# Performance work log

Hardware: AMD Instinct MI355X
Metric: run time of the kernel (lower is better)

The kernel has to match this reference:

```python
import jax, jax.numpy as jnp
import numpy as np
import math

N, E, C, A, M, B, H = 50000, 600000, 32, 32, 32, 10, 64


def setup_inputs() -> dict:
    key = jax.random.key(0)
    ks = jax.random.split(key, 14)
    f = jnp.float32
    node_input = jax.random.normal(ks[0], (N, C), f)
    node_attr = jax.random.normal(ks[1], (N, A), f)
    node_deg = 1.0 + 31.0 * jax.random.uniform(ks[2], (N, 1), dtype=f)  # degrees >= 1
    edge_src = jax.random.randint(ks[3], (E,), 0, N, jnp.int32)
    edge_dst = jax.random.randint(ks[4], (E,), 0, N, jnp.int32)
    edge_attr = jax.random.normal(ks[5], (E, 9), f)  # SH up to lmax=2: 1+3+5
    edge_length_embedded = jax.random.uniform(ks[6], (E, B), dtype=f)
    w_lin_in = jax.random.normal(ks[7], (C, A, C), f)    # FCTP(Cx0e, Ax0e -> Cx0e)
    w_lin_mask = jax.random.normal(ks[8], (C, A, M), f)  # FCTP scalar block of linear_mask
    w_out0 = jax.random.normal(ks[9], (C, A, M), f)      # linear_output, l=0 block
    w_out1 = jax.random.normal(ks[10], (C, A, M), f)     # l=1 block
    w_out2 = jax.random.normal(ks[11], (C, A, M), f)     # l=2 block
    W0 = jax.random.normal(ks[12], (B, H), f)            # radial net (edge2weight)
    W1 = jax.random.normal(ks[13], (H, 3 * C), f)        # -> tensor_edge.weight_numel = 3C ('uvu', v=1)
    return dict(node_input=node_input, node_attr=node_attr, node_deg=node_deg,
                edge_src=edge_src, edge_dst=edge_dst, edge_attr=edge_attr,
                edge_length_embedded=edge_length_embedded,
                w_lin_in=w_lin_in, w_lin_mask=w_lin_mask,
                w_out0=w_out0, w_out1=w_out1, w_out2=w_out2, W0=W0, W1=W1,
                numb=100, n=8)


def reference(node_input, node_attr, node_deg, edge_src, edge_dst, edge_attr,
              edge_length_embedded, w_lin_in, w_lin_mask, w_out0, w_out1, w_out2,
              W0, W1, numb, n):
    # GraphConvolution.forward with irreps_in=Cx0e, irreps_node_attr=Ax0e,
    # irreps_edge_attr=1x0e+1x1o+1x2e (lmax=2), irreps_out=Mx0e+Mx1o+Mx2e.
    nN = node_input.shape[0]
    inv_ca = 1.0 / math.sqrt(C * A)

    def fctp_scalar(x, z, w):  # FullyConnectedTensorProduct with all-scalar in1/in2
        return jnp.einsum('nu,nv,uvk->nk', x, z, w) * inv_ca

    # linear_input, then node_deg normalization
    h0 = fctp_scalar(node_input, node_attr, w_lin_in)            # [N, C]
    deg_isqrt = 1.0 / jnp.sqrt(node_deg)                          # [N, 1]
    nf = h0 * deg_isqrt
    # linear_mask: only 0e outputs have tp paths (scalars x scalars); 1o/2e are zero
    mask_scalar = fctp_scalar(node_input, node_attr, w_lin_mask)  # [N, M]

    # edge2weight radial MLP (e3nn FullyConnectedNet style: /sqrt(fan_in), silu hidden)
    h = jax.nn.silu(edge_length_embedded @ W0 * (1.0 / math.sqrt(B)))
    ew = h @ W1 * (1.0 / math.sqrt(H))                            # [E, 3C]
    w0e, w1o, w2e = ew[:, :C], ew[:, C:2 * C], ew[:, 2 * C:]

    # tensor_edge: 'uvu' 0e(x)l->l paths: out[u,m] = w[u]*x_src[u]*Y_l[m]
    xs = nf[edge_src]                                             # gather [E, C]
    m0 = (w0e * xs) * edge_attr[:, :1]                            # [E, C]
    m1 = (w1o * xs)[:, :, None] * edge_attr[:, None, 1:4]         # [E, C, 3]
    m2 = (w2e * xs)[:, :, None] * edge_attr[:, None, 4:9]         # [E, C, 5]

    # scatter-reduce to destination nodes, then deg normalization
    a0 = jax.ops.segment_sum(m0, edge_dst, num_segments=nN) * deg_isqrt
    a1 = jax.ops.segment_sum(m1, edge_dst, num_segments=nN) * deg_isqrt[:, :, None]
    a2 = jax.ops.segment_sum(m2, edge_dst, num_segments=nN) * deg_isqrt[:, :, None]

    # linear_output: FCTP(mid, Ax0e -> out); scalar attr mixes multiplicities per l
    out0 = jnp.einsum('nu,nv,uvk->nk', a0, node_attr, w_out0) * inv_ca        # [N, M]
    out1 = jnp.einsum('num,nv,uvk->nkm', a1, node_attr, w_out1) * inv_ca      # [N, M, 3]
    out2 = jnp.einsum('num,nv,uvk->nkm', a2, node_attr, w_out2) * inv_ca      # [N, M, 5]

    # c_s * node_mask + c_x * node_output; output_mask is 1 on 0e, 0 on 1o/2e
    c_s, c_x = math.sin(math.pi / 8), math.cos(math.pi / 8)
    scal = c_s * mask_scalar + c_x * out0
    return jnp.concatenate([scal, out1.reshape(nN, 3 * M), out2.reshape(nN, 5 * M)], axis=1)
```

## Files before the change

### kernel.cpp

```cpp
#include <hip/hip_runtime.h>

#define NC 32
#define NA 32
#define NB 10
#define NH 64

typedef __attribute__((ext_vector_type(8))) short bf16x8;
typedef __attribute__((ext_vector_type(4))) float f32x4;

static __device__ __forceinline__ unsigned short f2bf(float f) {
  union { float f; unsigned u; } v; v.f = f;
  unsigned r = v.u + 0x7fffu + ((v.u >> 16) & 1u);
  return (unsigned short)(r >> 16);
}
static __device__ __forceinline__ float bf2f(unsigned short b) {
  union { unsigned u; float f; } v; v.u = ((unsigned)b) << 16;
  return v.f;
}

__global__ void k_prep(const float* __restrict__ nattr, const float* __restrict__ ndeg,
                       const float* __restrict__ w0, const float* __restrict__ w1,
                       const float* __restrict__ w2, const float* __restrict__ w3,
                       const float* __restrict__ w4, const float* __restrict__ W1g,
                       unsigned short* __restrict__ zb, float* __restrict__ dis,
                       unsigned short* __restrict__ wrp, unsigned short* __restrict__ w1p,
                       int N) {
  int i = blockIdx.x * 256 + threadIdx.x;
  int nz = N * NC;
  if (i < nz) { zb[i] = f2bf(nattr[i]); return; }
  i -= nz;
  if (i < N) { dis[i] = rsqrtf(ndeg[i]); return; }
  i -= N;
  if (i < 5 * 32768) {
    int T = i >> 15, r = i & 32767;
    int t = r >> 9, l = (r >> 3) & 63, b = r & 7;
    int j = t * 16 + (l & 15);
    int u = j >> 5, k = j & 31, v = 8 * (l >> 4) + b;
    const float* w = (T == 0) ? w0 : (T == 1) ? w1 : (T == 2) ? w2 : (T == 3) ? w3 : w4;
    wrp[T * 32768 + (t * 64 + l) * 8 + b] = f2bf(w[u * 1024 + v * 32 + k] * (1.0f / 32.0f));
    return;
  }
  i -= 5 * 32768;
  if (i < 6144) {
    int c = i / 3072, r2 = i % 3072;
    int t = r2 >> 9, l = (r2 >> 3) & 63, b = r2 & 7;
    int k = 32 * c + 8 * (l >> 4) + b, col = 16 * t + (l & 15);
    w1p[i] = f2bf(W1g[k * 96 + col] * 0.125f);
  }
}

__global__ __launch_bounds__(512) void k_fctp(
    const unsigned short* __restrict__ wrp, const unsigned short* __restrict__ zb,
    const float* __restrict__ xp, int nm, int xnstr, int xoff,
    float* __restrict__ outp, int onstr,
    const float* __restrict__ scalep,
    const float* __restrict__ addp, float selfc, float addc) {
  __shared__ float zw[16 * 1025];
  __shared__ float xl[16][5][32];
  int tid = threadIdx.x;
  int lane = tid & 63, wv = tid >> 6;
  int nbase = blockIdx.x << 4;

  for (int i = tid; i < 16 * nm * 32; i += 512) {
    int n = i / (nm * 32); int rem = i - n * (nm * 32); int m = rem >> 5, u = rem & 31;
    xl[n][m][u] = xp[(nbase + n) * xnstr + xoff + m * 32 + u];
  }

  bf16x8 af = *(const bf16x8*)(zb + (nbase + (lane & 15)) * 32 + 8 * (lane >> 4));
  f32x4 acc[8];
#pragma unroll
  for (int i2 = 0; i2 < 8; ++i2) {
    int t = wv * 8 + i2;
    bf16x8 bfr = *(const bf16x8*)(wrp + (t * 64 + lane) * 8);
    f32x4 z4 = {0.f, 0.f, 0.f, 0.f};
    acc[i2] = __builtin_amdgcn_mfma_f32_16x16x32_bf16(af, bfr, z4, 0, 0, 0);
  }
  int rb = 4 * (lane >> 4);
#pragma unroll
  for (int i2 = 0; i2 < 8; ++i2) {
    int col = (wv * 8 + i2) * 16 + (lane & 15);
#pragma unroll
    for (int r = 0; r < 4; ++r) zw[(rb + r) * 1025 + col] = acc[i2][r];
  }
  __syncthreads();

  int n = tid >> 5, k = tid & 31;
  float sc = scalep ? scalep[nbase + n] : 1.0f;
  const float* zr = &zw[n * 1025];
  for (int m = 0; m < nm; ++m) {
    float s = 0.f;
#pragma unroll
    for (int u = 0; u < 32; ++u) s = fmaf(xl[n][m][u], zr[u * 32 + k], s);
    s *= sc;
    if (addp) s = selfc * s + addc * addp[(nbase + n) * 32 + k];
    outp[(nbase + n) * onstr + k * nm + m] = s;
  }
}

__global__ void k_count(const int* __restrict__ dst, int* __restrict__ cnt, int E) {
  int i = blockIdx.x * 256 + threadIdx.x;
  if (i < E) atomicAdd(&cnt[dst[i]], 1);
}
__global__ __launch_bounds__(512) void k_scan1(const int* __restrict__ cnt, int* __restrict__ exl,
                                               int* __restrict__ bsum, int n) {
  __shared__ int s[512];
  int t = threadIdx.x;
  int i = blockIdx.x * 512 + t;
  int v = (i < n) ? cnt[i] : 0;
  s[t] = v;
  __syncthreads();
  for (int off = 1; off < 512; off <<= 1) {
    int add = (t >= off) ? s[t - off] : 0;
    __syncthreads();
    s[t] += add;
    __syncthreads();
  }
  if (i < n) exl[i] = s[t] - v;
  if (t == 511) bsum[blockIdx.x] = s[511];
}
__global__ void k_scan2(int* __restrict__ bsum, int nb) {
  __shared__ int s[128];
  int t = threadIdx.x;
  int v = (t < nb) ? bsum[t] : 0;
  s[t] = v;
  __syncthreads();
  for (int off = 1; off < 128; off <<= 1) {
    int add = (t >= off) ? s[t - off] : 0;
    __syncthreads();
    s[t] += add;
    __syncthreads();
  }
  if (t < nb) bsum[t] = s[t] - v;
}
__global__ void k_scan3(int* __restrict__ off, const int* __restrict__ bbase,
                        int* __restrict__ cur, int N, int E) {
  int i = blockIdx.x * 256 + threadIdx.x;
  if (i < N) {
    int o = off[i] + bbase[i >> 9];
    off[i] = o;
    cur[i] = o;
  } else if (i == N) {
    off[N] = E;
  }
}
__global__ void k_fill(const int* __restrict__ dst, int* __restrict__ cur,
                       int* __restrict__ eid, int E) {
  int i = blockIdx.x * 256 + threadIdx.x;
  if (i < E) {
    int pos = atomicAdd(&cur[dst[i]], 1);
    eid[pos] = i;
  }
}

__global__ __launch_bounds__(256) void k_mlp(const float* __restrict__ el,
                                             const float* __restrict__ W0g,
                                             const unsigned short* __restrict__ w1p,
                                             unsigned short* __restrict__ ew, int E) {
  __shared__ float w0s[NB * NH];
  int tid = threadIdx.x;
  for (int i = tid; i < NB * NH; i += 256) w0s[i] = W0g[i] * 0.31622776601683794f;
  __syncthreads();
  int lane = tid & 63, wv = tid >> 6;
  int ebase = blockIdx.x * 64 + wv * 16;
  int erow = ebase + (lane & 15);
  float elr[NB];
#pragma unroll
  for (int b = 0; b < NB; ++b) elr[b] = el[erow * NB + b];
  int g8 = 8 * (lane >> 4);
  bf16x8 afr[2];
#pragma unroll
  for (int c = 0; c < 2; ++c) {
#pragma unroll
    for (int b = 0; b < 8; ++b) {
      int j = 32 * c + g8 + b;
      float p = 0.f;
#pragma unroll
      for (int q = 0; q < NB; ++q) p = fmaf(elr[q], w0s[q * NH + j], p);
      float h = p / (1.f + __expf(-p));
      afr[c][b] = (short)f2bf(h);
    }
  }
  f32x4 acc[6];
#pragma unroll
  for (int t = 0; t < 6; ++t) { f32x4 z4 = {0.f, 0.f, 0.f, 0.f}; acc[t] = z4; }
#pragma unroll
  for (int c = 0; c < 2; ++c) {
#pragma unroll
    for (int t = 0; t < 6; ++t) {
      bf16x8 bfr = *(const bf16x8*)(w1p + ((c * 6 + t) * 64 + lane) * 8);
      acc[t] = __builtin_amdgcn_mfma_f32_16x16x32_bf16(afr[c], bfr, acc[t], 0, 0, 0);
    }
  }
  int rb = 4 * (lane >> 4);
#pragma unroll
  for (int t = 0; t < 6; ++t) {
    int col = 16 * t + (lane & 15);
#pragma unroll
    for (int r = 0; r < 4; ++r) {
      int e = ebase + rb + r;
      ew[e * 96 + col] = f2bf(acc[t][r]);
    }
  }
}

__global__ __launch_bounds__(256) void k_gather(
    const int* __restrict__ off, const int* __restrict__ eid, const int* __restrict__ esrc,
    const float* __restrict__ eattr, const unsigned short* __restrict__ ew,
    const float* __restrict__ nf, const float* __restrict__ dis,
    float* __restrict__ a_all, int N) {
  int hw = (blockIdx.x * 256 + threadIdx.x) >> 5;
  int u = threadIdx.x & 31;
  if (hw >= N) return;
  int beg = off[hw], end = off[hw + 1];
  float a0 = 0, a1x = 0, a1y = 0, a1z = 0, b0 = 0, b1 = 0, b2 = 0, b3 = 0, b4 = 0;
  for (int p = beg; p < end; ++p) {
    int e = eid[p];
    int s = esrc[e];
    float xs = nf[s * 32 + u];
    const unsigned short* ewr = ew + e * 96;
    float w0 = bf2f(ewr[u]), w1 = bf2f(ewr[32 + u]), w2 = bf2f(ewr[64 + u]);
    const float* ea = eattr + e * 9;
    float t0 = w0 * xs, t1 = w1 * xs, t2 = w2 * xs;
    a0  = fmaf(t0, ea[0], a0);
    a1x = fmaf(t1, ea[1], a1x);
    a1y = fmaf(t1, ea[2], a1y);
    a1z = fmaf(t1, ea[3], a1z);
    b0  = fmaf(t2, ea[4], b0);
    b1  = fmaf(t2, ea[5], b1);
    b2  = fmaf(t2, ea[6], b2);
    b3  = fmaf(t2, ea[7], b3);
    b4  = fmaf(t2, ea[8], b4);
  }
  float d = dis[hw];
  float* ar = a_all + hw * 288;
  ar[0 * 32 + u] = a0 * d;
  ar[1 * 32 + u] = a1x * d;
  ar[2 * 32 + u] = a1y * d;
  ar[3 * 32 + u] = a1z * d;
  ar[4 * 32 + u] = b0 * d;
  ar[5 * 32 + u] = b1 * d;
  ar[6 * 32 + u] = b2 * d;
  ar[7 * 32 + u] = b3 * d;
  ar[8 * 32 + u] = b4 * d;
}

extern "C" void kernel_launch(void* const* d_in, const int* in_sizes, int n_in,
                              void* d_out, int out_size, void* d_ws, size_t ws_size,
                              hipStream_t stream) {
  const float* node_input = (const float*)d_in[0];
  const float* node_attr  = (const float*)d_in[1];
  const float* node_deg   = (const float*)d_in[2];
  const int*   edge_src   = (const int*)d_in[3];
  const int*   edge_dst   = (const int*)d_in[4];
  const float* edge_attr  = (const float*)d_in[5];
  const float* el_emb     = (const float*)d_in[6];
  const float* w_lin_in   = (const float*)d_in[7];
  const float* w_lin_mask = (const float*)d_in[8];
  const float* w_out0     = (const float*)d_in[9];
  const float* w_out1     = (const float*)d_in[10];
  const float* w_out2     = (const float*)d_in[11];
  const float* W0         = (const float*)d_in[12];
  const float* W1         = (const float*)d_in[13];
  int N = in_sizes[0] / 32;
  int E = in_sizes[3];
  float* out = (float*)d_out;

  char* p = (char*)d_ws;
  auto carve = [&](size_t bytes) { char* r = p; p += (bytes + 255) & ~(size_t)255; return r; };
  unsigned short* ew  = (unsigned short*)carve((size_t)E * 96 * 2);
  float* a_all        = (float*)carve((size_t)N * 288 * 4);
  float* nf           = (float*)carve((size_t)N * 32 * 4);
  float* maskb        = (float*)carve((size_t)N * 32 * 4);
  unsigned short* zb  = (unsigned short*)carve((size_t)N * 32 * 2);
  float* dis          = (float*)carve((size_t)N * 4);
  unsigned short* wrp = (unsigned short*)carve(5 * 32768 * 2);
  unsigned short* w1p = (unsigned short*)carve(6144 * 2);
  int* cnt            = (int*)carve((size_t)N * 4);
  int* off            = (int*)carve((size_t)(N + 1) * 4);
  int* cur            = (int*)carve((size_t)N * 4);
  int* eid            = (int*)carve((size_t)E * 4);
  int* bsum           = (int*)carve(1024);

  hipMemsetAsync(cnt, 0, (size_t)N * 4, stream);

  int tot = N * 32 + N + 5 * 32768 + 6144;
  k_prep<<<(tot + 255) / 256, 256, 0, stream>>>(node_attr, node_deg, w_lin_in, w_lin_mask,
                                                w_out0, w_out1, w_out2, W1, zb, dis, wrp, w1p, N);

  const float c_s = 0.3826834323650898f;
  const float c_x = 0.9238795325112867f;
  int nblk = N / 16;

  k_fctp<<<nblk, 512, 0, stream>>>(wrp + 0 * 32768, zb, node_input, 1, 32, 0, nf, 32,
                                   dis, nullptr, 0.f, 0.f);
  k_fctp<<<nblk, 512, 0, stream>>>(wrp + 1 * 32768, zb, node_input, 1, 32, 0, maskb, 32,
                                   nullptr, nullptr, 0.f, 0.f);

  k_count<<<(E + 255) / 256, 256, 0, stream>>>(edge_dst, cnt, E);
  int nb1 = (N + 511) / 512;
  k_scan1<<<nb1, 512, 0, stream>>>(cnt, off, bsum, N);
  k_scan2<<<1, 128, 0, stream>>>(bsum, nb1);
  k_scan3<<<(N + 1 + 255) / 256, 256, 0, stream>>>(off, bsum, cur, N, E);
  k_fill<<<(E + 255) / 256, 256, 0, stream>>>(edge_dst, cur, eid, E);

  k_mlp<<<E / 64, 256, 0, stream>>>(el_emb, W0, w1p, ew, E);
  k_gather<<<(N * 32 + 255) / 256, 256, 0, stream>>>(off, eid, edge_src, edge_attr, ew, nf,
                                                     dis, a_all, N);

  k_fctp<<<nblk, 512, 0, stream>>>(wrp + 2 * 32768, zb, a_all, 1, 288, 0, out + 0, 288,
                                   nullptr, maskb, c_x, c_s);
  k_fctp<<<nblk, 512, 0, stream>>>(wrp + 3 * 32768, zb, a_all, 3, 288, 32, out + 32, 288,
                                   nullptr, nullptr, 0.f, 0.f);
  k_fctp<<<nblk, 512, 0, stream>>>(wrp + 4 * 32768, zb, a_all, 5, 288, 128, out + 128, 288,
                                   nullptr, nullptr, 0.f, 0.f);
}
```

Before: 456.4 us.

## Scatter edge weights and attributes into CSR order in MLP kernel

The fill kernel now records each edge's CSR position, and the edge MLP kernel stages its bf16 output in shared memory before writing it, together with edge_src and edge_attr, into dst-sorted order. The gather kernel then reads edge data contiguously by CSR position instead of through an indirection, and it also prefetches the next source node feature. This removes the random eid-indexed loads from the gather at the cost of scattered writes in the MLP kernel and extra workspace for the permuted edge_src and edge_attr arrays.

After: 488.6 us. 1.07x slower.

```diff
diff --git a/kernel.cpp b/kernel.cpp
--- a/kernel.cpp
+++ b/kernel.cpp
@@ -144,25 +144,42 @@
   }
 }
 __global__ void k_fill(const int* __restrict__ dst, int* __restrict__ cur,
-                       int* __restrict__ eid, int E) {
+                       int* __restrict__ pos, int E) {
   int i = blockIdx.x * 256 + threadIdx.x;
   if (i < E) {
-    int pos = atomicAdd(&cur[dst[i]], 1);
-    eid[pos] = i;
+    pos[i] = atomicAdd(&cur[dst[i]], 1);
   }
 }
 
 __global__ __launch_bounds__(256) void k_mlp(const float* __restrict__ el,
                                              const float* __restrict__ W0g,
                                              const unsigned short* __restrict__ w1p,
-                                             unsigned short* __restrict__ ew, int E) {
+                                             const int* __restrict__ pos,
+                                             const int* __restrict__ esrc,
+                                             const float* __restrict__ eattr,
+                                             unsigned short* __restrict__ ewP,
+                                             int* __restrict__ esrcP,
+                                             float* __restrict__ eattrP, int E) {
   __shared__ float w0s[NB * NH];
+  __shared__ __align__(16) unsigned short tile[64 * 104];
+  __shared__ int posl[64];
   int tid = threadIdx.x;
+  int ebase = blockIdx.x * 64;
   for (int i = tid; i < NB * NH; i += 256) w0s[i] = W0g[i] * 0.31622776601683794f;
-  __syncthreads();
+  if (tid < 64) posl[tid] = pos[ebase + tid];
+  __syncthreads();
+
+  for (int i = tid; i < 64 * 10; i += 256) {
+    int le = i / 10, c = i - le * 10;
+    int p = posl[le];
+    int e = ebase + le;
+    if (c == 0) esrcP[p] = esrc[e];
+    else eattrP[(size_t)p * 9 + (c - 1)] = eattr[(size_t)e * 9 + (c - 1)];
+  }
+
   int lane = tid & 63, wv = tid >> 6;
-  int ebase = blockIdx.x * 64 + wv * 16;
-  int erow = ebase + (lane & 15);
+  int eloc0 = wv * 16;
+  int erow = ebase + eloc0 + (lane & 15);
   float elr[NB];
 #pragma unroll
   for (int b = 0; b < NB; ++b) elr[b] = el[erow * NB + b];
@@ -197,15 +214,21 @@
     int col = 16 * t + (lane & 15);
 #pragma unroll
     for (int r = 0; r < 4; ++r) {
-      int e = ebase + rb + r;
-      ew[e * 96 + col] = f2bf(acc[t][r]);
+      tile[(eloc0 + rb + r) * 104 + col] = f2bf(acc[t][r]);
     }
   }
+  __syncthreads();
+  for (int ch = tid; ch < 64 * 12; ch += 256) {
+    int le = ch / 12, seg = ch - le * 12;
+    int p = posl[le];
+    *(uint4*)(ewP + (size_t)p * 96 + seg * 8) =
+        *(const uint4*)(&tile[le * 104 + seg * 8]);
+  }
 }
 
 __global__ __launch_bounds__(256) void k_gather(
-    const int* __restrict__ off, const int* __restrict__ eid, const int* __restrict__ esrc,
-    const float* __restrict__ eattr, const unsigned short* __restrict__ ew,
+    const int* __restrict__ off, const int* __restrict__ esrcP,
+    const float* __restrict__ eattrP, const unsigned short* __restrict__ ewP,
     const float* __restrict__ nf, const float* __restrict__ dis,
     float* __restrict__ a_all, int N) {
   int hw = (blockIdx.x * 256 + threadIdx.x) >> 5;
@@ -213,13 +236,20 @@
   if (hw >= N) return;
   int beg = off[hw], end = off[hw + 1];
   float a0 = 0, a1x = 0, a1y = 0, a1z = 0, b0 = 0, b1 = 0, b2 = 0, b3 = 0, b4 = 0;
+  float xs_next = 0.f;
+  if (beg < end) {
+    int s0 = esrcP[beg];
+    xs_next = nf[(size_t)s0 * 32 + u];
+  }
   for (int p = beg; p < end; ++p) {
-    int e = eid[p];
-    int s = esrc[e];
-    float xs = nf[s * 32 + u];
-    const unsigned short* ewr = ew + e * 96;
+    float xs = xs_next;
+    if (p + 1 < end) {
+      int s2 = esrcP[p + 1];
+      xs_next = nf[(size_t)s2 * 32 + u];
+    }
+    const unsigned short* ewr = ewP + (size_t)p * 96;
     float w0 = bf2f(ewr[u]), w1 = bf2f(ewr[32 + u]), w2 = bf2f(ewr[64 + u]);
-    const float* ea = eattr + e * 9;
+    const float* ea = eattrP + (size_t)p * 9;
     float t0 = w0 * xs, t1 = w1 * xs, t2 = w2 * xs;
     a0  = fmaf(t0, ea[0], a0);
     a1x = fmaf(t1, ea[1], a1x);
@@ -232,7 +262,7 @@
     b4  = fmaf(t2, ea[8], b4);
   }
   float d = dis[hw];
-  float* ar = a_all + hw * 288;
+  float* ar = a_all + (size_t)hw * 288;
   ar[0 * 32 + u] = a0 * d;
   ar[1 * 32 + u] = a1x * d;
   ar[2 * 32 + u] = a1y * d;
@@ -268,6 +298,8 @@
   char* p = (char*)d_ws;
   auto carve = [&](size_t bytes) { char* r = p; p += (bytes + 255) & ~(size_t)255; return r; };
   unsigned short* ew  = (unsigned short*)carve((size_t)E * 96 * 2);
+  float* eattrP       = (float*)carve((size_t)E * 9 * 4);
+  int* esrcP          = (int*)carve((size_t)E * 4);
   float* a_all        = (float*)carve((size_t)N * 288 * 4);
   float* nf           = (float*)carve((size_t)N * 32 * 4);
   float* maskb        = (float*)carve((size_t)N * 32 * 4);
@@ -278,7 +310,7 @@
   int* cnt            = (int*)carve((size_t)N * 4);
   int* off            = (int*)carve((size_t)(N + 1) * 4);
   int* cur            = (int*)carve((size_t)N * 4);
-  int* eid            = (int*)carve((size_t)E * 4);
+  int* pos            = (int*)carve((size_t)E * 4);
   int* bsum           = (int*)carve(1024);
 
   hipMemsetAsync(cnt, 0, (size_t)N * 4, stream);
@@ -301,10 +333,11 @@
   k_scan1<<<nb1, 512, 0, stream>>>(cnt, off, bsum, N);
   k_scan2<<<1, 128, 0, stream>>>(bsum, nb1);
   k_scan3<<<(N + 1 + 255) / 256, 256, 0, stream>>>(off, bsum, cur, N, E);
-  k_fill<<<(E + 255) / 256, 256, 0, stream>>>(edge_dst, cur, eid, E);
-
-  k_mlp<<<E / 64, 256, 0, stream>>>(el_emb, W0, w1p, ew, E);
-  k_gather<<<(N * 32 + 255) / 256, 256, 0, stream>>>(off, eid, edge_src, edge_attr, ew, nf,
+  k_fill<<<(E + 255) / 256, 256, 0, stream>>>(edge_dst, cur, pos, E);
+
+  k_mlp<<<E / 64, 256, 0, stream>>>(el_emb, W0, w1p, pos, edge_src, edge_attr,
+                                    ew, esrcP, eattrP, E);
+  k_gather<<<(N * 32 + 255) / 256, 256, 0, stream>>>(off, esrcP, eattrP, ew, nf,
                                                      dis, a_all, N);
 
   k_fctp<<<nblk, 512, 0, stream>>>(wrp + 2 * 32768, zb, a_all, 1, 288, 0, out + 0, 288,
```
